# Performance work log

Hardware: AMD Instinct MI355X
Metric: run time of the kernel (lower is better)

The kernel has to match this reference:

```python
import jax, jax.numpy as jnp
import numpy as np

H = 8        # attention heads
TOP_K = 2    # gating top-k
STEPS = 5    # dream_length


def _layernorm(x, w, b, eps=1e-5):
    m = jnp.mean(x, axis=-1, keepdims=True)
    v = jnp.var(x, axis=-1, keepdims=True)
    return (x - m) * jax.lax.rsqrt(v + eps) * w + b


def _mha(x, in_w, in_b, out_w, out_b):
    # torch nn.MultiheadAttention (batch_first, self-attention, eval mode)
    Bx, T, Dm = x.shape
    hd = Dm // H
    qkv = x @ in_w.T + in_b                      # (B, T, 3D)
    q, k, v = jnp.split(qkv, 3, axis=-1)
    sh = lambda t: t.reshape(Bx, T, H, hd).transpose(0, 2, 1, 3)
    q, k, v = sh(q), sh(k), sh(v)
    a = jax.nn.softmax(jnp.einsum('bhqd,bhkd->bhqk', q, k) / np.sqrt(hd).astype(np.float32), axis=-1)
    o = jnp.einsum('bhqk,bhkd->bhqd', a, v).transpose(0, 2, 1, 3).reshape(Bx, T, Dm)
    return o @ out_w.T + out_b


def _triplet_proj(p, x):
    xn = _layernorm(x, p['tln_w'], p['tln_b'])
    h = jax.nn.gelu(xn @ p['tw1'].T + p['tb1'], approximate=False)
    return h @ p['tw2'].T + p['tb2']


def _dream_sequence(p, triplet):
    # triplet: (Bt, 3, D); returns (STEPS, 3, Bt, D)
    Bt, _, Dm = triplet.shape
    seq = [jnp.mean(triplet, axis=1)]
    n_layers = p['an_w'].shape[0]
    for step in range(STEPS):
        st = jnp.stack(seq, axis=1) + p['pos'][:step + 1]   # (Bt, t, D)
        for l in range(n_layers):
            xn = _layernorm(st, p['an_w'][l], p['an_b'][l])
            st = st + _mha(xn, p['in_w'][l], p['in_b'][l], p['ow'][l], p['ob'][l])
            fn = _layernorm(st, p['fn_w'][l], p['fn_b'][l])
            st = st + jax.nn.gelu(fn @ p['w1'][l].T + p['b1'][l], approximate=False) @ p['w2'][l].T + p['b2'][l]
        nxt = _triplet_proj(p, st[:, -1]).reshape(Bt, 3, Dm).mean(axis=1)
        seq.append(nxt)
    embs = jnp.stack(seq[1:], axis=0)                        # (STEPS, Bt, D)
    trip = _triplet_proj(p, embs).reshape(STEPS, Bt, 3, Dm)
    return trip.transpose(0, 2, 1, 3)


def _forward(initial_what, initial_action, initial_result, dream_offsets,
             gw1, gb1, gln_w, gln_b, gw2, gb2,
             pos, an_w, an_b, in_w, in_b, ow, ob, fn_w, fn_b, w1, b1, w2, b2,
             tln_w, tln_b, tw1, tb1, tw2, tb2):
    B, Dm = initial_what.shape
    ND = dream_offsets.shape[0]
    triplet = jnp.stack([initial_what, initial_action, initial_result], axis=1)  # (B, 3, D)
    # --- noisy top-k gating (eval mode: no noise, no dropout) ---
    flat = triplet.reshape(B, 3 * Dm)
    g = jax.nn.gelu(_layernorm(flat @ gw1.T + gb1, gln_w, gln_b), approximate=False)
    logits = g @ gw2.T + gb2                                 # (B, E)
    tv, ti = jax.lax.top_k(logits, TOP_K)
    gates = jax.nn.softmax(tv, axis=-1)
    weights = jnp.zeros_like(logits).at[jnp.arange(B)[:, None], ti].set(gates)
    # --- diversified starts; fold dreams into batch ---
    big = (triplet[None] + dream_offsets[:, None]).reshape(ND * B, 3, Dm)
    ep = dict(pos=pos, an_w=an_w, an_b=an_b, in_w=in_w, in_b=in_b, ow=ow, ob=ob,
              fn_w=fn_w, fn_b=fn_b, w1=w1, b1=b1, w2=w2, b2=b2,
              tln_w=tln_w, tln_b=tln_b, tw1=tw1, tb1=tb1, tw2=tw2, tb2=tb2)
    expert_out = jax.vmap(lambda p: _dream_sequence(p, big))(ep)   # (E, STEPS, 3, ND*B, D)
    E = logits.shape[1]
    expert_out = expert_out.reshape(E, STEPS, 3, ND, B, Dm)
    # weighted combine over experts -> (num_dreams, dream_length, 3, B, D)
    return jnp.einsum('estnbd,be->nstbd', expert_out, weights)


def setup_inputs() -> dict:
    D, E, L, FF, B, ND = 1024, 4, 2, 4096, 512, 3
    ks = iter(jax.random.split(jax.random.key(0), 16))
    nrm = lambda shape, s=1.0: jax.random.normal(next(ks), shape, jnp.float32) * s
    return dict(
        initial_what=nrm((B, D)), initial_action=nrm((B, D)), initial_result=nrm((B, D)),
        dream_offsets=nrm((ND, 3, D), 0.1),
        gw1=nrm((D, 3 * D), (3 * D) ** -0.5), gb1=jnp.zeros((D,)),
        gln_w=jnp.ones((D,)), gln_b=jnp.zeros((D,)),
        gw2=nrm((E, D), D ** -0.5), gb2=jnp.zeros((E,)),
        pos=nrm((E, 10, D)),
        an_w=jnp.ones((E, L, D)), an_b=jnp.zeros((E, L, D)),
        in_w=nrm((E, L, 3 * D, D), D ** -0.5), in_b=jnp.zeros((E, L, 3 * D)),
        ow=nrm((E, L, D, D), D ** -0.5), ob=jnp.zeros((E, L, D)),
        fn_w=jnp.ones((E, L, D)), fn_b=jnp.zeros((E, L, D)),
        w1=nrm((E, L, FF, D), D ** -0.5), b1=jnp.zeros((E, L, FF)),
        w2=nrm((E, L, D, FF), FF ** -0.5), b2=jnp.zeros((E, L, D)),
        tln_w=jnp.ones((E, D)), tln_b=jnp.zeros((E, D)),
        tw1=nrm((E, 2 * D, D), D ** -0.5), tb1=jnp.zeros((E, 2 * D)),
        tw2=nrm((E, 3 * D, 2 * D), (2 * D) ** -0.5), tb2=jnp.zeros((E, 3 * D)),
    )


def reference(initial_what, initial_action, initial_result, dream_offsets,
              gw1, gb1, gln_w, gln_b, gw2, gb2,
              pos, an_w, an_b, in_w, in_b, ow, ob, fn_w, fn_b, w1, b1, w2, b2,
              tln_w, tln_b, tw1, tb1, tw2, tb2):
    return _forward(initial_what, initial_action, initial_result, dream_offsets,
                    gw1, gb1, gln_w, gln_b, gw2, gb2,
                    pos, an_w, an_b, in_w, in_b, ow, ob, fn_w, fn_b, w1, b1, w2, b2,
                    tln_w, tln_b, tw1, tb1, tw2, tb2)
```

## Files before the change

kernel.cpp:

```cpp
#include <hip/hip_runtime.h>
#include <hip/hip_bf16.h>
#include <cstdint>

#define B_  512
#define D_  1024
#define E_  4
#define L_  2
#define FF_ 4096
#define ND_ 3
#define BT_ 1536
#define STEPS_ 5
#define H_ 8
#define PROWS 3584
#define TROWS (PROWS * STEPS_)

typedef __attribute__((ext_vector_type(8))) __bf16 bf16x8;
typedef __attribute__((ext_vector_type(8))) unsigned short u16x8;
typedef __attribute__((ext_vector_type(4))) float f32x4;

static __device__ __forceinline__ float gelu_f(float x) {
    return 0.5f * x * (1.0f + erff(x * 0.70710678118654752f));
}

static __device__ __forceinline__ unsigned short f2bf(float x) {
    unsigned u = __builtin_bit_cast(unsigned, x);
    u = (u + 0x7fff + ((u >> 16) & 1)) >> 16;
    return (unsigned short)u;
}

static __device__ __forceinline__ float bf2f(unsigned short us) {
    unsigned v = (unsigned)us << 16;
    return __builtin_bit_cast(float, v);
}

static __device__ __forceinline__ void gload16(const void* g, void* l) {
    __builtin_amdgcn_global_load_lds(
        (const __attribute__((address_space(1))) unsigned int*)g,
        (__attribute__((address_space(3))) unsigned int*)l, 16, 0, 0);
}

static __device__ __forceinline__ int pad128(int x) { return (x + 127) & ~127; }

template<int ACT, int OUTBF>
__global__ __launch_bounds__(512) void gemm_wf32(
    const unsigned short* __restrict__ A,
    const float* __restrict__ Wb, long wstride, int LDA,
    const float* __restrict__ biasb, long bstride,
    const float* __restrict__ R, long Rld, void* __restrict__ Cout, int N, int K,
    const int* __restrict__ roff, int T)
{
    const long row0 = (long)blockIdx.y * 128;
    if ((int)row0 >= roff[4] * T) return;
    int e = 0;
    while (e < 3 && (int)row0 >= roff[e + 1] * T) ++e;
    const float* W = Wb + (long)e * wstride;
    const float* bias = biasb ? (biasb + (long)e * bstride) : nullptr;

    __shared__ __align__(16) unsigned short As[2 * 128 * 32];
    __shared__ __align__(16) unsigned short Bs[2 * 128 * 32];
    const int t = threadIdx.x;
    const int lane = t & 63;
    const int wid = t >> 6;
    const int wr = wid >> 1;
    const int wc = wid & 1;
    const long col0 = (long)blockIdx.x * 128;
    const int l15 = lane & 15, l4 = lane >> 4;

    f32x4 acc[2][4] = {};

    const unsigned short* Ag = A + (row0 + (t >> 2)) * (long)K + (t & 3) * 8;
    char* AdBase = (char*)As + t * 16;

    const float* Wg = W + (long)(col0 + (t >> 2)) * LDA + (t & 3) * 8;

    const int K32 = K >> 5;
    float4 w0, w1;

    gload16(Ag, AdBase);
    w0 = *(const float4*)(Wg);
    w1 = *(const float4*)(Wg + 4);
    {
        u16x8 p = {f2bf(w0.x), f2bf(w0.y), f2bf(w0.z), f2bf(w0.w),
                   f2bf(w1.x), f2bf(w1.y), f2bf(w1.z), f2bf(w1.w)};
        *(u16x8*)((char*)Bs + t * 16) = p;
    }
    if (K32 > 1) {
        w0 = *(const float4*)(Wg + 32);
        w1 = *(const float4*)(Wg + 36);
    }
    __syncthreads();

    for (int j = 0; j < K32; ++j) {
        const int cur = j & 1;
        const int nxt = cur ^ 1;
        if (j + 1 < K32) {
            gload16(Ag + ((j + 1) << 5), AdBase + nxt * 8192);
            u16x8 p = {f2bf(w0.x), f2bf(w0.y), f2bf(w0.z), f2bf(w0.w),
                       f2bf(w1.x), f2bf(w1.y), f2bf(w1.z), f2bf(w1.w)};
            *(u16x8*)((char*)Bs + nxt * 8192 + t * 16) = p;
        }
        if (j + 2 < K32) {
            const int k2 = (j + 2) << 5;
            w0 = *(const float4*)(Wg + k2);
            w1 = *(const float4*)(Wg + k2 + 4);
        }
        bf16x8 af[2], bf[4];
        #pragma unroll
        for (int m = 0; m < 2; ++m)
            af[m] = *(const bf16x8*)((const char*)As + cur * 8192 + (wr * 32 + m * 16 + l15) * 64 + l4 * 16);
        #pragma unroll
        for (int n = 0; n < 4; ++n)
            bf[n] = *(const bf16x8*)((const char*)Bs + cur * 8192 + (wc * 64 + n * 16 + l15) * 64 + l4 * 16);
        #pragma unroll
        for (int m = 0; m < 2; ++m)
            #pragma unroll
            for (int n = 0; n < 4; ++n)
                acc[m][n] = __builtin_amdgcn_mfma_f32_16x16x32_bf16(af[m], bf[n], acc[m][n], 0, 0, 0);
        __syncthreads();
    }

    #pragma unroll
    for (int n = 0; n < 4; ++n) {
        const long col = col0 + wc * 64 + n * 16 + l15;
        const float bn = bias ? bias[col] : 0.0f;
        #pragma unroll
        for (int m = 0; m < 2; ++m) {
            const long rbase = row0 + wr * 32 + m * 16 + l4 * 4;
            #pragma unroll
            for (int r = 0; r < 4; ++r) {
                float o = acc[m][n][r] + bn;
                if (ACT) o = gelu_f(o);
                const long coff = (rbase + r) * (long)N + col;
                if (R) o += R[(rbase + r) * Rld + col];
                if (OUTBF) ((unsigned short*)Cout)[coff] = f2bf(o);
                else       ((float*)Cout)[coff] = o;
            }
        }
    }
}

__global__ __launch_bounds__(256) void gemm_f32(
    const float* __restrict__ A, const float* __restrict__ W,
    const float* __restrict__ bias, const float* __restrict__ R,
    float* __restrict__ C, int M, int N, int K, int act)
{
    __shared__ float As[16][68];
    __shared__ float Bs[16][68];
    const int tid = threadIdx.x;
    const int tx = tid & 15;
    const int ty = tid >> 4;
    const long row0 = (long)blockIdx.y * 64;
    const long col0 = (long)blockIdx.x * 64;
    const int lr = tid >> 2;
    const int lq = (tid & 3) << 2;
    const float* Ap = A + (row0 + lr) * (long)K + lq;
    const float* Wp = W + (col0 + lr) * (long)K + lq;
    float acc[4][4] = {};
    for (int k0 = 0; k0 < K; k0 += 16) {
        const float4 av = *(const float4*)(Ap + k0);
        const float4 wv = *(const float4*)(Wp + k0);
        __syncthreads();
        As[lq + 0][lr] = av.x; As[lq + 1][lr] = av.y;
        As[lq + 2][lr] = av.z; As[lq + 3][lr] = av.w;
        Bs[lq + 0][lr] = wv.x; Bs[lq + 1][lr] = wv.y;
        Bs[lq + 2][lr] = wv.z; Bs[lq + 3][lr] = wv.w;
        __syncthreads();
        #pragma unroll
        for (int kk = 0; kk < 16; ++kk) {
            const float4 a4 = *(const float4*)&As[kk][ty << 2];
            const float4 b4 = *(const float4*)&Bs[kk][tx << 2];
            const float aa[4] = {a4.x, a4.y, a4.z, a4.w};
            const float bb[4] = {b4.x, b4.y, b4.z, b4.w};
            #pragma unroll
            for (int i = 0; i < 4; ++i)
                #pragma unroll
                for (int j = 0; j < 4; ++j)
                    acc[i][j] = fmaf(aa[i], bb[j], acc[i][j]);
        }
    }
    const float4 bv = *(const float4*)(bias + col0 + (tx << 2));
    const float bb[4] = {bv.x, bv.y, bv.z, bv.w};
    #pragma unroll
    for (int i = 0; i < 4; ++i) {
        const long row = row0 + (ty << 2) + i;
        const long off = row * (long)N + col0 + (tx << 2);
        float o[4];
        #pragma unroll
        for (int j = 0; j < 4; ++j) {
            o[j] = acc[i][j] + bb[j];
            if (act) o[j] = gelu_f(o[j]);
        }
        if (R) {
            const float4 rv = *(const float4*)(R + off);
            o[0] += rv.x; o[1] += rv.y; o[2] += rv.z; o[3] += rv.w;
        }
        *(float4*)(C + off) = make_float4(o[0], o[1], o[2], o[3]);
    }
}

__global__ __launch_bounds__(256) void ln_gate(
    const float* __restrict__ X,
    const float* __restrict__ gamma, const float* __restrict__ beta,
    float* __restrict__ Y)
{
    const long r = blockIdx.x;
    const int tid = threadIdx.x;
    __shared__ float red[8];
    const float4 v = *(const float4*)(X + (r << 10) + (tid << 2));
    float s = v.x + v.y + v.z + v.w;
    #pragma unroll
    for (int off = 32; off; off >>= 1) s += __shfl_xor(s, off);
    if ((tid & 63) == 0) red[tid >> 6] = s;
    __syncthreads();
    const float mean = (red[0] + red[1] + red[2] + red[3]) * (1.0f / 1024.0f);
    const float dx = v.x - mean, dy = v.y - mean, dz = v.z - mean, dw = v.w - mean;
    float s2 = dx * dx + dy * dy + dz * dz + dw * dw;
    #pragma unroll
    for (int off = 32; off; off >>= 1) s2 += __shfl_xor(s2, off);
    if ((tid & 63) == 0) red[4 + (tid >> 6)] = s2;
    __syncthreads();
    const float var = (red[4] + red[5] + red[6] + red[7]) * (1.0f / 1024.0f);
    const float inv = rsqrtf(var + 1e-5f);
    const float4 g = *(const float4*)(gamma + (tid << 2));
    const float4 b = *(const float4*)(beta + (tid << 2));
    float o0 = gelu_f(dx * inv * g.x + b.x);
    float o1 = gelu_f(dy * inv * g.y + b.y);
    float o2 = gelu_f(dz * inv * g.z + b.z);
    float o3 = gelu_f(dw * inv * g.w + b.w);
    *(float4*)(Y + (r << 10) + (tid << 2)) = make_float4(o0, o1, o2, o3);
}

__global__ __launch_bounds__(256) void ln_bt(
    const float* __restrict__ X, long xstride,
    const float* __restrict__ gammaB, const float* __restrict__ betaB, long gstride,
    unsigned short* __restrict__ Y, const int* __restrict__ roff, int T)
{
    const long r = blockIdx.x;
    if ((int)r >= roff[4] * T) return;
    int e = 0;
    while (e < 3 && (int)r >= roff[e + 1] * T) ++e;
    const float* gamma = gammaB + (long)e * gstride;
    const float* beta  = betaB  + (long)e * gstride;

    const int tid = threadIdx.x;
    __shared__ float red[8];
    const float4 v = *(const float4*)(X + r * xstride + (tid << 2));
    float s = v.x + v.y + v.z + v.w;
    #pragma unroll
    for (int off = 32; off; off >>= 1) s += __shfl_xor(s, off);
    if ((tid & 63) == 0) red[tid >> 6] = s;
    __syncthreads();
    const float mean = (red[0] + red[1] + red[2] + red[3]) * (1.0f / 1024.0f);
    const float dx = v.x - mean, dy = v.y - mean, dz = v.z - mean, dw = v.w - mean;
    float s2 = dx * dx + dy * dy + dz * dz + dw * dw;
    #pragma unroll
    for (int off = 32; off; off >>= 1) s2 += __shfl_xor(s2, off);
    if ((tid & 63) == 0) red[4 + (tid >> 6)] = s2;
    __syncthreads();
    const float var = (red[4] + red[5] + red[6] + red[7]) * (1.0f / 1024.0f);
    const float inv = rsqrtf(var + 1e-5f);
    const float4 g = *(const float4*)(gamma + (tid << 2));
    const float4 b = *(const float4*)(beta + (tid << 2));
    const float o0 = dx * inv * g.x + b.x;
    const float o1 = dy * inv * g.y + b.y;
    const float o2 = dz * inv * g.z + b.z;
    const float o3 = dw * inv * g.w + b.w;
    ushort4 o = make_ushort4(f2bf(o0), f2bf(o1), f2bf(o2), f2bf(o3));
    *(ushort4*)(Y + (r << 10) + (tid << 2)) = o;
}

template<int TT>
__global__ __launch_bounds__(256) void attn_bt(
    const unsigned short* __restrict__ qkv, unsigned short* __restrict__ o,
    const int* __restrict__ roff)
{
    const int item = (int)(((long)blockIdx.x * 256 + threadIdx.x) >> 6);
    const int lane = threadIdx.x & 63;
    const int tq = item % TT;
    const int h  = (item / TT) & 7;
    const int i  = item / (TT * 8);
    if (i >= roff[4]) return;
    const unsigned short* base = qkv + (long)i * TT * 3072;
    const unsigned short* q = base + (long)tq * 3072 + h * 128;
    const float q0 = bf2f(q[lane]), q1 = bf2f(q[lane + 64]);
    float s[TT];
    const float scale = 0.088388347648318447f;
    #pragma unroll
    for (int tk = 0; tk < TT; ++tk) {
        const unsigned short* k = base + (long)tk * 3072 + 1024 + h * 128;
        float p = q0 * bf2f(k[lane]) + q1 * bf2f(k[lane + 64]);
        #pragma unroll
        for (int off = 32; off; off >>= 1) p += __shfl_xor(p, off);
        s[tk] = p * scale;
    }
    float m = s[0];
    #pragma unroll
    for (int tk = 1; tk < TT; ++tk) m = fmaxf(m, s[tk]);
    float den = 0.f;
    #pragma unroll
    for (int tk = 0; tk < TT; ++tk) { s[tk] = expf(s[tk] - m); den += s[tk]; }
    float o0 = 0.f, o1 = 0.f;
    #pragma unroll
    for (int tk = 0; tk < TT; ++tk) {
        const unsigned short* v = base + (long)tk * 3072 + 2048 + h * 128;
        o0 += s[tk] * bf2f(v[lane]); o1 += s[tk] * bf2f(v[lane + 64]);
    }
    const float id = 1.0f / den;
    unsigned short* op = o + ((long)i * TT + tq) * 1024 + h * 128;
    op[lane] = f2bf(o0 * id); op[lane + 64] = f2bf(o1 * id);
}

template<int TT>
__global__ __launch_bounds__(256) void attn_last(
    const unsigned short* __restrict__ qkv, unsigned short* __restrict__ o,
    const int* __restrict__ roff)
{
    const int item = (int)(((long)blockIdx.x * 256 + threadIdx.x) >> 6);
    const int lane = threadIdx.x & 63;
    const int h  = item & 7;
    const int i  = item >> 3;
    if (i >= roff[4]) return;
    const unsigned short* base = qkv + (long)i * TT * 3072;
    const unsigned short* q = base + (long)(TT - 1) * 3072 + h * 128;
    const float q0 = bf2f(q[lane]), q1 = bf2f(q[lane + 64]);
    float s[TT];
    const float scale = 0.088388347648318447f;
    #pragma unroll
    for (int tk = 0; tk < TT; ++tk) {
        const unsigned short* k = base + (long)tk * 3072 + 1024 + h * 128;
        float p = q0 * bf2f(k[lane]) + q1 * bf2f(k[lane + 64]);
        #pragma unroll
        for (int off = 32; off; off >>= 1) p += __shfl_xor(p, off);
        s[tk] = p * scale;
    }
    float m = s[0];
    #pragma unroll
    for (int tk = 1; tk < TT; ++tk) m = fmaxf(m, s[tk]);
    float den = 0.f;
    #pragma unroll
    for (int tk = 0; tk < TT; ++tk) { s[tk] = expf(s[tk] - m); den += s[tk]; }
    float o0 = 0.f, o1 = 0.f;
    #pragma unroll
    for (int tk = 0; tk < TT; ++tk) {
        const unsigned short* v = base + (long)tk * 3072 + 2048 + h * 128;
        o0 += s[tk] * bf2f(v[lane]); o1 += s[tk] * bf2f(v[lane + 64]);
    }
    const float id = 1.0f / den;
    unsigned short* op = o + (long)i * 1024 + h * 128;
    op[lane] = f2bf(o0 * id); op[lane + 64] = f2bf(o1 * id);
}

__global__ __launch_bounds__(256) void gate_kernel(
    const float* __restrict__ g, const float* __restrict__ gw2,
    const float* __restrict__ gb2, float* __restrict__ wout)
{
    const int b = (int)(((long)blockIdx.x * 256 + threadIdx.x) >> 6);
    const int lane = threadIdx.x & 63;
    float acc[E_] = {};
    const float* row = g + (long)b * 1024;
    for (int d = lane; d < 1024; d += 64) {
        const float x = row[d];
        #pragma unroll
        for (int j = 0; j < E_; ++j) acc[j] += x * gw2[j * 1024 + d];
    }
    #pragma unroll
    for (int j = 0; j < E_; ++j) {
        #pragma unroll
        for (int off = 32; off; off >>= 1) acc[j] += __shfl_xor(acc[j], off);
        acc[j] += gb2[j];
    }
    int i0 = 0; float v0 = acc[0];
    #pragma unroll
    for (int j = 1; j < E_; ++j) if (acc[j] > v0) { v0 = acc[j]; i0 = j; }
    int i1 = -1; float v1 = -1e30f;
    #pragma unroll
    for (int j = 0; j < E_; ++j) if (j != i0 && acc[j] > v1) { v1 = acc[j]; i1 = j; }
    const float p1 = expf(v1 - v0);
    const float den = 1.0f + p1;
    const float g0 = 1.0f / den, g1 = p1 / den;
    if (lane < E_) wout[b * E_ + lane] = (lane == i0) ? g0 : (lane == i1) ? g1 : 0.0f;
}

__global__ __launch_bounds__(64) void build_idx2_kernel(
    const float* __restrict__ wbuf, int* __restrict__ idx,
    int* __restrict__ cnt3, int* __restrict__ roff)
{
    const int lane = threadIdx.x;
    int pads[E_];
    for (int e = 0; e < E_; ++e) {
        int* my = idx + e * BT_;
        int base = 0;
        for (int chunk = 0; chunk < 8; ++chunk) {
            const int b = chunk * 64 + lane;
            const bool sel = wbuf[b * E_ + e] > 0.0f;
            const unsigned long long mask = __ballot(sel);
            const int pos = base + (int)__popcll(mask & ((1ull << lane) - 1ull));
            if (sel) {
                my[3 * pos + 0] = b;
                my[3 * pos + 1] = 512 + b;
                my[3 * pos + 2] = 1024 + b;
            }
            base += (int)__popcll(mask);
        }
        if (lane == 0) cnt3[e] = 3 * base;
        pads[e] = pad128(3 * base);
    }
    if (lane == 0) {
        roff[0] = 0;
        for (int e = 0; e < E_; ++e) roff[e + 1] = roff[e] + pads[e];
    }
}

__global__ __launch_bounds__(256) void seq0_bt(
    const float* __restrict__ w, const float* __restrict__ a,
    const float* __restrict__ rr, const float* __restrict__ doff,
    const int* __restrict__ idx, const int* __restrict__ cnt3,
    const int* __restrict__ roff, float* __restrict__ seq0)
{
    const int prow = blockIdx.x;
    if (prow >= roff[4]) return;
    int e = 0;
    while (e < 3 && prow >= roff[e + 1]) ++e;
    const int j = prow - roff[e];
    const int d4 = threadIdx.x << 2;
    float4 res = make_float4(0.f, 0.f, 0.f, 0.f);
    if (j < cnt3[e]) {
        const int v = idx[e * BT_ + j];
        const int n = v >> 9, b = v & 511;
        const float4 x = *(const float4*)(w + ((long)b << 10) + d4);
        const float4 y = *(const float4*)(a + ((long)b << 10) + d4);
        const float4 z = *(const float4*)(rr + ((long)b << 10) + d4);
        const float4 o0 = *(const float4*)(doff + ((long)(n * 3 + 0) << 10) + d4);
        const float4 o1 = *(const float4*)(doff + ((long)(n * 3 + 1) << 10) + d4);
        const float4 o2 = *(const float4*)(doff + ((long)(n * 3 + 2) << 10) + d4);
        const float c = 1.0f / 3.0f;
        res = make_float4(
            (x.x + y.x + z.x + o0.x + o1.x + o2.x) * c,
            (x.y + y.y + z.y + o0.y + o1.y + o2.y) * c,
            (x.z + y.z + z.z + o0.z + o1.z + o2.z) * c,
            (x.w + y.w + z.w + o0.w + o1.w + o2.w) * c);
    }
    *(float4*)(seq0 + ((long)prow << 10) + d4) = res;
}

__global__ __launch_bounds__(256) void build_st_bt(
    const float* __restrict__ seq, const float* __restrict__ posb,
    float* __restrict__ st, int T, const int* __restrict__ roff)
{
    const int trow = blockIdx.x;
    const int prow = trow / T;
    if (prow >= roff[4]) return;
    int e = 0;
    while (e < 3 && prow >= roff[e + 1]) ++e;
    const int tau = trow - prow * T;
    const int d4 = threadIdx.x << 2;
    const float4 s = *(const float4*)(seq + (((long)tau * PROWS + prow) << 10) + d4);
    const float4 p = *(const float4*)(posb + (((long)e * 10 + tau) << 10) + d4);
    *(float4*)(st + ((long)trow << 10) + d4) = make_float4(s.x + p.x, s.y + p.y, s.z + p.z, s.w + p.w);
}

__global__ __launch_bounds__(256) void mean3_bt(
    const float* __restrict__ O, float* __restrict__ dst,
    const int* __restrict__ roff)
{
    const int r = blockIdx.x;
    if (r >= roff[4]) return;
    const int d4 = threadIdx.x << 2;
    const float* p = O + (long)r * 3072 + d4;
    const float4 x = *(const float4*)p;
    const float4 y = *(const float4*)(p + 1024);
    const float4 z = *(const float4*)(p + 2048);
    const float c = 1.0f / 3.0f;
    *(float4*)(dst + ((long)r << 10) + d4) = make_float4(
        (x.x + y.x + z.x) * c, (x.y + y.y + z.y) * c,
        (x.z + y.z + z.z) * c, (x.w + y.w + z.w) * c);
}

__global__ __launch_bounds__(256) void scatter_bt(
    const float* __restrict__ O, const float* __restrict__ wbuf,
    const int* __restrict__ idx, const int* __restrict__ cnt3,
    const int* __restrict__ roff, float* __restrict__ out, int e, int s)
{
    const int r = blockIdx.x;
    if (r >= cnt3[e]) return;
    const int prow = roff[e] + r;
    const int v = idx[e * BT_ + r];
    const int n = v >> 9, b = v & 511;
    const float wgt = wbuf[b * E_ + e];
    const int d4 = threadIdx.x << 2;
    const float* orow = O + (long)prow * 3072;
    #pragma unroll
    for (int c = 0; c < 3; ++c) {
        const float4 t = *(const float4*)(orow + c * 1024 + d4);
        float* op = out + (((long)((n * STEPS_ + s) * 3 + c) * B_ + b) << 10) + d4;
        float4 o = *(const float4*)op;
        o.x += wgt * t.x; o.y += wgt * t.y; o.z += wgt * t.z; o.w += wgt * t.w;
        *(float4*)op = o;
    }
}

__global__ __launch_bounds__(256) void build_flat_kernel(
    const float* __restrict__ w, const float* __restrict__ a,
    const float* __restrict__ r, float* __restrict__ flat)
{
    const long e4 = ((long)blockIdx.x * 256 + threadIdx.x) << 2;
    const int b = (int)(e4 / 3072);
    const int cd = (int)(e4 % 3072);
    const int c = cd >> 10, d = cd & 1023;
    const float* src = (c == 0) ? w : (c == 1) ? a : r;
    *(float4*)(flat + e4) = *(const float4*)(src + ((long)b << 10) + d);
}

__global__ __launch_bounds__(256) void zero_kernel(float* __restrict__ p, long n4)
{
    const long stride = (long)gridDim.x * 256;
    for (long i = (long)blockIdx.x * 256 + threadIdx.x; i < n4; i += stride)
        *(float4*)(p + i * 4) = make_float4(0.f, 0.f, 0.f, 0.f);
}


extern "C" void kernel_launch(void* const* d_in, const int* in_sizes, int n_in,
                              void* d_out, int out_size, void* d_ws, size_t ws_size,
                              hipStream_t stream)
{
    const float* iw   = (const float*)d_in[0];
    const float* ia   = (const float*)d_in[1];
    const float* ir   = (const float*)d_in[2];
    const float* doff = (const float*)d_in[3];
    const float* gw1  = (const float*)d_in[4];
    const float* gb1  = (const float*)d_in[5];
    const float* glnw = (const float*)d_in[6];
    const float* glnb = (const float*)d_in[7];
    const float* gw2  = (const float*)d_in[8];
    const float* gb2  = (const float*)d_in[9];
    const float* pos  = (const float*)d_in[10];
    const float* anw  = (const float*)d_in[11];
    const float* anb  = (const float*)d_in[12];
    const float* inw  = (const float*)d_in[13];
    const float* inb  = (const float*)d_in[14];
    const float* oww  = (const float*)d_in[15];
    const float* owb  = (const float*)d_in[16];
    const float* fnw  = (const float*)d_in[17];
    const float* fnb  = (const float*)d_in[18];
    const float* w1   = (const float*)d_in[19];
    const float* b1   = (const float*)d_in[20];
    const float* w2   = (const float*)d_in[21];
    const float* b2   = (const float*)d_in[22];
    const float* tlnw = (const float*)d_in[23];
    const float* tlnb = (const float*)d_in[24];
    const float* tw1  = (const float*)d_in[25];
    const float* tb1  = (const float*)d_in[26];
    const float* tw2  = (const float*)d_in[27];
    const float* tb2  = (const float*)d_in[28];
    float* out = (float*)d_out;

    float* ws    = (float*)d_ws;
    float* wbuf  = ws;
    int*   cnt3  = (int*)(wbuf + 2048);
    int*   roff  = cnt3 + 16;
    int*   idxb  = roff + 16;
    float* flatb = (float*)(idxb + 4 * BT_);
    float* glin  = flatb + (long)B_ * 3072;
    float* seq   = glin + (long)B_ * 1024;
    float* st    = seq + 6L * PROWS * 1024;
    unsigned short* xnB  = (unsigned short*)(st + (long)TROWS * 1024);
    unsigned short* bigB = xnB + (long)TROWS * 1024;
    unsigned short* Fbuf = bigB;
    unsigned short* axB  = xnB;
    float* Obuf = (float*)(bigB + 16777216);
    float* stL  = seq + 5L * PROWS * 1024;
    if (ws_size < 79175712UL * sizeof(float)) return;

    build_flat_kernel<<<B_ * 3, 256, 0, stream>>>(iw, ia, ir, flatb);
    gemm_f32<<<dim3(16, 8), 256, 0, stream>>>(flatb, gw1, gb1, nullptr, glin, B_, 1024, 3072, 0);
    ln_gate<<<B_, 256, 0, stream>>>(glin, glnw, glnb, glin);
    gate_kernel<<<B_ / 4, 256, 0, stream>>>(glin, gw2, gb2, wbuf);
    build_idx2_kernel<<<1, 64, 0, stream>>>(wbuf, idxb, cnt3, roff);

    zero_kernel<<<2048, 256, 0, stream>>>(out, (long)ND_ * STEPS_ * 3 * B_ * 1024 / 4);

    seq0_bt<<<PROWS, 256, 0, stream>>>(iw, ia, ir, doff, idxb, cnt3, roff, seq);

    for (int t = 0; t < STEPS_; ++t) {
        const int T = t + 1;
        const int MT = PROWS * T;
        build_st_bt<<<MT, 256, 0, stream>>>(seq, pos, st, T, roff);

        {
            const int l = 0;
            ln_bt<<<MT, 256, 0, stream>>>(st, 1024, anw + l * 1024, anb + l * 1024,
                                          (long)L_ * 1024, xnB, roff, T);
            gemm_wf32<0, 1><<<dim3(24, MT / 128), 512, 0, stream>>>(
                xnB, inw + (long)l * 3072 * 1024, (long)L_ * 3072 * 1024, 1024,
                inb + l * 3072, (long)L_ * 3072, nullptr, 0, bigB, 3072, 1024, roff, T);
            switch (T) {
                case 1: attn_bt<1><<<PROWS * 8 * 1 / 4, 256, 0, stream>>>(bigB, xnB, roff); break;
                case 2: attn_bt<2><<<PROWS * 8 * 2 / 4, 256, 0, stream>>>(bigB, xnB, roff); break;
                case 3: attn_bt<3><<<PROWS * 8 * 3 / 4, 256, 0, stream>>>(bigB, xnB, roff); break;
                case 4: attn_bt<4><<<PROWS * 8 * 4 / 4, 256, 0, stream>>>(bigB, xnB, roff); break;
                case 5: attn_bt<5><<<PROWS * 8 * 5 / 4, 256, 0, stream>>>(bigB, xnB, roff); break;
            }
            gemm_wf32<0, 0><<<dim3(8, MT / 128), 512, 0, stream>>>(
                xnB, oww + (long)l * 1024 * 1024, (long)L_ * 1024 * 1024, 1024,
                owb + l * 1024, (long)L_ * 1024, st, 1024, st, 1024, 1024, roff, T);
            ln_bt<<<MT, 256, 0, stream>>>(st, 1024, fnw + l * 1024, fnb + l * 1024,
                                          (long)L_ * 1024, xnB, roff, T);
            for (int c = 0; c < 2; ++c) {
                gemm_wf32<1, 1><<<dim3(16, MT / 128), 512, 0, stream>>>(
                    xnB, w1 + (long)l * 4096 * 1024 + (long)c * 2048 * 1024,
                    (long)L_ * 4096 * 1024, 1024,
                    b1 + l * 4096 + c * 2048, (long)L_ * 4096, nullptr, 0, bigB, 2048, 1024, roff, T);
                gemm_wf32<0, 0><<<dim3(8, MT / 128), 512, 0, stream>>>(
                    bigB, w2 + (long)l * 1024 * 4096 + (long)c * 2048,
                    (long)L_ * 1024 * 4096, 4096,
                    (c == 0) ? (b2 + l * 1024) : nullptr, (long)L_ * 1024,
                    st, 1024, st, 1024, 2048, roff, T);
            }
        }

        {
            const int l = 1;
            ln_bt<<<MT, 256, 0, stream>>>(st, 1024, anw + l * 1024, anb + l * 1024,
                                          (long)L_ * 1024, xnB, roff, T);
            gemm_wf32<0, 1><<<dim3(24, MT / 128), 512, 0, stream>>>(
                xnB, inw + (long)l * 3072 * 1024, (long)L_ * 3072 * 1024, 1024,
                inb + l * 3072, (long)L_ * 3072, nullptr, 0, bigB, 3072, 1024, roff, T);
            switch (T) {
                case 1: attn_last<1><<<PROWS * 8 / 4, 256, 0, stream>>>(bigB, axB, roff); break;
                case 2: attn_last<2><<<PROWS * 8 / 4, 256, 0, stream>>>(bigB, axB, roff); break;
                case 3: attn_last<3><<<PROWS * 8 / 4, 256, 0, stream>>>(bigB, axB, roff); break;
                case 4: attn_last<4><<<PROWS * 8 / 4, 256, 0, stream>>>(bigB, axB, roff); break;
                case 5: attn_last<5><<<PROWS * 8 / 4, 256, 0, stream>>>(bigB, axB, roff); break;
            }
            gemm_wf32<0, 0><<<dim3(8, PROWS / 128), 512, 0, stream>>>(
                axB, oww + (long)l * 1024 * 1024, (long)L_ * 1024 * 1024, 1024,
                owb + l * 1024, (long)L_ * 1024,
                st + (long)t * 1024, (long)T * 1024, stL, 1024, 1024, roff, 1);
            ln_bt<<<PROWS, 256, 0, stream>>>(stL, 1024, fnw + l * 1024, fnb + l * 1024,
                                             (long)L_ * 1024, xnB, roff, 1);
            for (int c = 0; c < 2; ++c) {
                gemm_wf32<1, 1><<<dim3(16, PROWS / 128), 512, 0, stream>>>(
                    xnB, w1 + (long)l * 4096 * 1024 + (long)c * 2048 * 1024,
                    (long)L_ * 4096 * 1024, 1024,
                    b1 + l * 4096 + c * 2048, (long)L_ * 4096, nullptr, 0, Fbuf, 2048, 1024, roff, 1);
                gemm_wf32<0, 0><<<dim3(8, PROWS / 128), 512, 0, stream>>>(
                    Fbuf, w2 + (long)l * 1024 * 4096 + (long)c * 2048,
                    (long)L_ * 1024 * 4096, 4096,
                    (c == 0) ? (b2 + l * 1024) : nullptr, (long)L_ * 1024,
                    stL, 1024, stL, 1024, 2048, roff, 1);
            }
        }

        ln_bt<<<PROWS, 256, 0, stream>>>(stL, 1024, tlnw, tlnb, 1024, xnB, roff, 1);
        gemm_wf32<1, 1><<<dim3(16, PROWS / 128), 512, 0, stream>>>(
            xnB, tw1, 2048L * 1024, 1024, tb1, 2048, nullptr, 0, Fbuf, 2048, 1024, roff, 1);
        gemm_wf32<0, 0><<<dim3(24, PROWS / 128), 512, 0, stream>>>(
            Fbuf, tw2, 3072L * 2048, 2048, tb2, 3072, nullptr, 0, Obuf, 3072, 2048, roff, 1);
        mean3_bt<<<PROWS, 256, 0, stream>>>(Obuf, seq + (long)(t + 1) * PROWS * 1024, roff);
    }
    for (int s = 0; s < STEPS_; ++s) {
        ln_bt<<<PROWS, 256, 0, stream>>>(seq + (long)(s + 1) * PROWS * 1024, 1024,
                                         tlnw, tlnb, 1024, xnB, roff, 1);
        gemm_wf32<1, 1><<<dim3(16, PROWS / 128), 512, 0, stream>>>(
            xnB, tw1, 2048L * 1024, 1024, tb1, 2048, nullptr, 0, Fbuf, 2048, 1024, roff, 1);
        gemm_wf32<0, 0><<<dim3(24, PROWS / 128), 512, 0, stream>>>(
            Fbuf, tw2, 3072L * 2048, 2048, tb2, 3072, nullptr, 0, Obuf, 3072, 2048, roff, 1);
        for (int e = 0; e < E_; ++e)
            scatter_bt<<<BT_, 256, 0, stream>>>(Obuf, wbuf, idxb, cnt3, roff, out, e, s);
    }
}
```

Baseline: 6.933 ms.

## Triple-buffer GEMM shared tiles with XOR swizzle and single barrier per step

Moves the fp32-weight GEMM from double to triple buffering in LDS. Each K step now uses one barrier, guarded by explicit vmcnt/lgkmcnt waits, so global loads for step j+2 can run while step j computes. It also XOR-swizzles the 16-byte chunks in the A and B tiles to reduce LDS bank conflicts on the MFMA fragment reads. The cost is 50% more shared memory per block and a hand-counted vmcnt value that depends on how the compiler orders the loads.

```diff
diff --git a/kernel.cpp b/kernel.cpp
--- a/kernel.cpp
+++ b/kernel.cpp
@@ -56,8 +56,8 @@
     const float* W = Wb + (long)e * wstride;
     const float* bias = biasb ? (biasb + (long)e * bstride) : nullptr;
 
-    __shared__ __align__(16) unsigned short As[2 * 128 * 32];
-    __shared__ __align__(16) unsigned short Bs[2 * 128 * 32];
+    __shared__ __align__(16) unsigned short As[3 * 128 * 32];
+    __shared__ __align__(16) unsigned short Bs[3 * 128 * 32];
     const int t = threadIdx.x;
     const int lane = t & 63;
     const int wid = t >> 6;
@@ -65,58 +65,71 @@
     const int wc = wid & 1;
     const long col0 = (long)blockIdx.x * 128;
     const int l15 = lane & 15, l4 = lane >> 4;
+    const int rsw = l15 & 3;
 
     f32x4 acc[2][4] = {};
 
-    const unsigned short* Ag = A + (row0 + (t >> 2)) * (long)K + (t & 3) * 8;
-    char* AdBase = (char*)As + t * 16;
-
-    const float* Wg = W + (long)(col0 + (t >> 2)) * LDA + (t & 3) * 8;
+    const int arow = t >> 2;
+    const int achk = (t & 3) ^ (arow & 3);
+    const unsigned short* Ag = A + (row0 + arow) * (long)K + achk * 8;
+    char* Aslot = (char*)As + t * 16;
+    const float* Wg = W + (long)(col0 + arow) * LDA + (t & 3) * 8;
+    const int wdst = (arow << 6) + (((t & 3) ^ (arow & 3)) << 4);
 
     const int K32 = K >> 5;
     float4 w0, w1;
-
-    gload16(Ag, AdBase);
+    float4 v0, v1;
+
     w0 = *(const float4*)(Wg);
     w1 = *(const float4*)(Wg + 4);
+    gload16(Ag, Aslot);
+    if (K32 > 1) {
+        v0 = *(const float4*)(Wg + 32);
+        v1 = *(const float4*)(Wg + 36);
+        gload16(Ag + 32, Aslot + 8192);
+    }
     {
         u16x8 p = {f2bf(w0.x), f2bf(w0.y), f2bf(w0.z), f2bf(w0.w),
                    f2bf(w1.x), f2bf(w1.y), f2bf(w1.z), f2bf(w1.w)};
-        *(u16x8*)((char*)Bs + t * 16) = p;
-    }
-    if (K32 > 1) {
-        w0 = *(const float4*)(Wg + 32);
-        w1 = *(const float4*)(Wg + 36);
-    }
-    __syncthreads();
+        *(u16x8*)((char*)Bs + wdst) = p;
+    }
+    w0 = v0; w1 = v1;
 
     for (int j = 0; j < K32; ++j) {
-        const int cur = j & 1;
-        const int nxt = cur ^ 1;
         if (j + 1 < K32) {
-            gload16(Ag + ((j + 1) << 5), AdBase + nxt * 8192);
+            asm volatile("s_waitcnt vmcnt(3) lgkmcnt(0)" ::: "memory");
+        } else {
+            asm volatile("s_waitcnt vmcnt(0) lgkmcnt(0)" ::: "memory");
+        }
+        __builtin_amdgcn_s_barrier();
+        __builtin_amdgcn_sched_barrier(0);
+
+        if (j + 2 < K32) {
+            const int k2 = (j + 2) << 5;
+            v0 = *(const float4*)(Wg + k2);
+            v1 = *(const float4*)(Wg + k2 + 4);
+            gload16(Ag + k2, Aslot + ((j + 2) % 3) * 8192);
+        }
+        if (j + 1 < K32) {
             u16x8 p = {f2bf(w0.x), f2bf(w0.y), f2bf(w0.z), f2bf(w0.w),
                        f2bf(w1.x), f2bf(w1.y), f2bf(w1.z), f2bf(w1.w)};
-            *(u16x8*)((char*)Bs + nxt * 8192 + t * 16) = p;
-        }
-        if (j + 2 < K32) {
-            const int k2 = (j + 2) << 5;
-            w0 = *(const float4*)(Wg + k2);
-            w1 = *(const float4*)(Wg + k2 + 4);
-        }
+            *(u16x8*)((char*)Bs + ((j + 1) % 3) * 8192 + wdst) = p;
+            w0 = v0; w1 = v1;
+        }
+        const char* Abase = (const char*)As + (j % 3) * 8192;
+        const char* Bbase = (const char*)Bs + (j % 3) * 8192;
         bf16x8 af[2], bf[4];
         #pragma unroll
         for (int m = 0; m < 2; ++m)
-            af[m] = *(const bf16x8*)((const char*)As + cur * 8192 + (wr * 32 + m * 16 + l15) * 64 + l4 * 16);
+            af[m] = *(const bf16x8*)(Abase + (wr * 32 + m * 16 + l15) * 64 + ((l4 ^ rsw) << 4));
         #pragma unroll
         for (int n = 0; n < 4; ++n)
-            bf[n] = *(const bf16x8*)((const char*)Bs + cur * 8192 + (wc * 64 + n * 16 + l15) * 64 + l4 * 16);
+            bf[n] = *(const bf16x8*)(Bbase + (wc * 64 + n * 16 + l15) * 64 + ((l4 ^ rsw) << 4));
         #pragma unroll
         for (int m = 0; m < 2; ++m)
             #pragma unroll
             for (int n = 0; n < 4; ++n)
                 acc[m][n] = __builtin_amdgcn_mfma_f32_16x16x32_bf16(af[m], bf[n], acc[m][n], 0, 0, 0);
-        __syncthreads();
     }
 
     #pragma unroll
```

Measured after the change: 8.353 ms. 1.2x slower.
